# Performance work log

Measured on AMD Instinct MI355X. Metric: run time of the kernel, lower is better.

The kernel has to match this reference:

```python
import jax, jax.numpy as jnp
import numpy as np

B, V, F = 64, 100000, 200000


def setup_inputs() -> dict:
    key = jax.random.key(0)
    k1, k2 = jax.random.split(key)
    verts = jax.random.normal(k1, (B, V, 3), dtype=jnp.float32)
    faces = jax.random.randint(k2, (F, 3), 0, V, dtype=jnp.int64)
    return {"verts": verts, "faces": faces}


def reference(verts, faces):
    # Directed edge list from triangles: each face (i,j,k) contributes
    # edges i<->j, j<->k, k<->i (with multiplicity), shape [6F].
    i, j, k = faces[:, 0], faces[:, 1], faces[:, 2]
    src = jnp.concatenate([i, j, j, k, k, i])
    dst = jnp.concatenate([j, i, k, j, i, k])

    nv = verts.shape[1]
    # Degree (neighbor count) per vertex; guard isolated vertices.
    deg = jnp.zeros((nv,), verts.dtype).at[src].add(1.0)
    deg = jnp.maximum(deg, 1.0)

    # Sum of neighbor positions via scatter-add: [B, V, 3]
    nbr_sum = jnp.zeros_like(verts).at[:, src].add(verts[:, dst])

    # Graph Laplacian: x - mean(neighbors)
    Lx = verts - nbr_sum / deg[None, :, None]

    # Per-vertex L2 norm, then mean over batch and vertices (scalar loss).
    per_vert = jnp.sqrt(jnp.sum(Lx * Lx, axis=-1))
    return per_vert.mean()
```

## Files before the change

### kernel.cpp

```cpp
#include <hip/hip_runtime.h>


#define BB 64
#define VV 100000
#define VP1 (VV + 1)
#define FF 200000
#define BUILD_BLOCKS ((FF + 255) / 256)
#define TR_BLOCKS ((VV + 63) / 64)
#define VBLK ((VV + 255) / 256)
#define NCHUNK (VV / 32)
#define SCALE 80.0f
#define BIAS_W ((512u) | (512u << 10) | (512u << 20))

#define WS_GHIST (448u * 1024u)
#define WS_GCUR (448u * 1024u + 128u)
#define WS_SLOTS (512u * 1024u)
#define WS_VPERM (14u * 1024u * 1024u)
#define WS_T (16u * 1024u * 1024u)

__device__ __forceinline__ int quant10(float x) {
    int qi = (int)rintf(x * SCALE);
    qi = min(max(qi, -511), 511);
    return qi + 512;
}

__global__ __launch_bounds__(256) void build_transpose_kernel(
    const float* __restrict__ verts, const int* __restrict__ faces,
    int* __restrict__ count, int* __restrict__ slots,
    unsigned int* __restrict__ T10) {
    __shared__ unsigned int lds32[64 * 100];
    if (blockIdx.x < BUILD_BLOCKS) {
        int f = blockIdx.x * 256 + threadIdx.x;
        if (f < FF) {
            int i = faces[3 * f + 0];
            int j = faces[3 * f + 1];
            int k = faces[3 * f + 2];
            int p;
            p = atomicAdd(count + i, 2);
            if (p + 1 < 32) *(int2*)(slots + ((size_t)i << 5) + p) = make_int2(j, k);
            p = atomicAdd(count + j, 2);
            if (p + 1 < 32) *(int2*)(slots + ((size_t)j << 5) + p) = make_int2(i, k);
            p = atomicAdd(count + k, 2);
            if (p + 1 < 32) *(int2*)(slots + ((size_t)k << 5) + p) = make_int2(i, j);
        }
    } else {
        int v0 = (blockIdx.x - BUILD_BLOCKS) * 64;
        int nv = min(64, VV - v0);
        int nf = 3 * nv;
        if (blockIdx.x == BUILD_BLOCKS && threadIdx.x < 64) {
            int g = threadIdx.x >> 3, bp = threadIdx.x & 7;
            T10[((size_t)g * VP1 + VV) * 8 + bp] = BIAS_W;
        }
        #pragma unroll
        for (int it = 0; it < 12; ++it) {
            int idx = it * 256 + threadIdx.x;
            int b = idx / 48;
            int q = idx - b * 48;
            if (4 * q < nf) {
                const float4 f4 =
                    *(const float4*)(verts + (size_t)b * (VV * 3) + (size_t)v0 * 3 + 4 * q);
                unsigned int u0 = (unsigned)quant10(f4.x);
                unsigned int u1 = (unsigned)quant10(f4.y);
                unsigned int u2 = (unsigned)quant10(f4.z);
                unsigned int u3 = (unsigned)quant10(f4.w);
                uint2 d;
                d.x = u0 | (u1 << 16);
                d.y = u2 | (u3 << 16);
                *(uint2*)&lds32[b * 100 + 2 * q] = d;
            }
        }
        __syncthreads();
        #pragma unroll
        for (int it = 0; it < 16; ++it) {
            int idx = it * 256 + threadIdx.x;
            int g = idx >> 9;
            int rem = idx & 511;
            int vloc = rem >> 3;
            int bp = rem & 7;
            if (vloc < nv) {
                int b = g * 8 + bp;
                int p0 = 3 * vloc;
                unsigned int dlo = lds32[b * 100 + (p0 >> 1)];
                unsigned int dhi = lds32[b * 100 + ((p0 + 2) >> 1)];
                unsigned long long pair = ((unsigned long long)dhi << 32) | dlo;
                pair >>= 16 * (p0 & 1);
                unsigned int u0 = (unsigned int)(pair & 1023u);
                unsigned int u1 = (unsigned int)((pair >> 16) & 1023u);
                unsigned int u2 = (unsigned int)((pair >> 32) & 1023u);
                T10[((size_t)g * VP1 + v0 + vloc) * 8 + bp] = u0 | (u1 << 10) | (u2 << 20);
            }
        }
    }
}

__global__ __launch_bounds__(256) void hist_kernel(const int* __restrict__ count,
                                                   int* __restrict__ ghist) {
    __shared__ int h[17];
    if (threadIdx.x < 17) h[threadIdx.x] = 0;
    __syncthreads();
    int v = blockIdx.x * 256 + threadIdx.x;
    if (v < VV) atomicAdd(&h[min(count[v], 32) >> 1], 1);
    __syncthreads();
    if (threadIdx.x < 17 && h[threadIdx.x]) atomicAdd(&ghist[threadIdx.x], h[threadIdx.x]);
}

__global__ void scan17_kernel(const int* __restrict__ ghist, int* __restrict__ gcur) {
    if (threadIdx.x == 0) {
        int run = 0;
        for (int u = 0; u < 17; ++u) {
            gcur[u] = run;
            run += ghist[u];
        }
    }
}

__global__ __launch_bounds__(256) void scatter_kernel(const int* __restrict__ count,
                                                      int* __restrict__ gcur,
                                                      unsigned int* __restrict__ vperm) {
    __shared__ int h[17], base[17];
    if (threadIdx.x < 17) h[threadIdx.x] = 0;
    __syncthreads();
    int v = blockIdx.x * 256 + threadIdx.x;
    int u = 0, lpos = 0, deg = 0;
    if (v < VV) {
        deg = count[v];
        u = min(deg, 32) >> 1;
        lpos = atomicAdd(&h[u], 1);
    }
    __syncthreads();
    if (threadIdx.x < 17 && h[threadIdx.x])
        base[threadIdx.x] = atomicAdd(&gcur[threadIdx.x], h[threadIdx.x]);
    __syncthreads();
    if (v < VV)
        vperm[base[u] + lpos] = (unsigned)v | ((unsigned)min(deg, 2047) << 20);
}

__inline__ __device__ float waveReduceSumF(float val) {
    #pragma unroll
    for (int o = 32; o > 0; o >>= 1) val += __shfl_down(val, o, 64);
    return val;
}

#define ACC(col, w)                       \
    {                                     \
        sx##col += (int)((w) & 1023u);    \
        sy##col += (int)(((w) >> 10) & 1023u); \
        sz##col += (int)((w) >> 20);      \
    }

#define LOSSC(col, w)                                            \
    {                                                            \
        float ax = (float)((int)((w) & 1023u) - 512);            \
        float ay = (float)((int)(((w) >> 10) & 1023u) - 512);    \
        float az = (float)((int)((w) >> 20) - 512);              \
        float lx = ax - ((float)sx##col - corr) * invd;          \
        float ly = ay - ((float)sy##col - corr) * invd;          \
        float lz = az - ((float)sz##col - corr) * invd;          \
        acc += sqrtf(lx * lx + ly * ly + lz * lz);               \
    }

__global__ __launch_bounds__(256) void loss_kernel(
    const unsigned int* __restrict__ T10, const unsigned int* __restrict__ vperm,
    const int* __restrict__ slots, float* __restrict__ out) {
    int lane = threadIdx.x & 63;
    int half = lane & 1;
    int vg = lane >> 1;
    int g = blockIdx.x & 7;
    const unsigned int* Tg = T10 + (size_t)g * VP1 * 8;
    int wis = ((blockIdx.x >> 3) << 2) + (threadIdx.x >> 6);
    float acc = 0.f;
    #pragma unroll 1
    for (int k = 0; k < 3; ++k) {
        int c = wis + k * 1044;
        if (c >= NCHUNK) break;
        unsigned int entry = vperm[c * 32 + vg];
        int v = (int)(entry & 0xFFFFFu);
        int deg = (int)(entry >> 20);
        int use = min(deg, 32);
        int mu = use;
        mu = max(mu, __shfl_xor(mu, 2, 64));
        mu = max(mu, __shfl_xor(mu, 4, 64));
        mu = max(mu, __shfl_xor(mu, 8, 64));
        mu = max(mu, __shfl_xor(mu, 16, 64));
        mu = max(mu, __shfl_xor(mu, 32, 64));
        mu = __builtin_amdgcn_readfirstlane(mu);
        int mu4 = (mu + 3) & ~3;
        const int* row = slots + ((size_t)v << 5);
        uint4 selfw = *(const uint4*)(Tg + ((size_t)v << 3) + (half << 2));
        int sx0 = 0, sy0 = 0, sz0 = 0, sx1 = 0, sy1 = 0, sz1 = 0;
        int sx2 = 0, sy2 = 0, sz2 = 0, sx3 = 0, sy3 = 0, sz3 = 0;
        for (int t = 0; t < mu4; t += 4) {
            int2 p01 = *(const int2*)(row + t);
            int2 p23 = *(const int2*)(row + t + 2);
            int n0 = (t + 0 < use) ? p01.x : VV;
            int n1 = (t + 1 < use) ? p01.y : VV;
            int n2 = (t + 2 < use) ? p23.x : VV;
            int n3 = (t + 3 < use) ? p23.y : VV;
            uint4 w0 = *(const uint4*)(Tg + ((size_t)n0 << 3) + (half << 2));
            uint4 w1 = *(const uint4*)(Tg + ((size_t)n1 << 3) + (half << 2));
            uint4 w2 = *(const uint4*)(Tg + ((size_t)n2 << 3) + (half << 2));
            uint4 w3 = *(const uint4*)(Tg + ((size_t)n3 << 3) + (half << 2));
            ACC(0, w0.x) ACC(1, w0.y) ACC(2, w0.z) ACC(3, w0.w)
            ACC(0, w1.x) ACC(1, w1.y) ACC(2, w1.z) ACC(3, w1.w)
            ACC(0, w2.x) ACC(1, w2.y) ACC(2, w2.z) ACC(3, w2.w)
            ACC(0, w3.x) ACC(1, w3.y) ACC(2, w3.z) ACC(3, w3.w)
        }
        float corr = 512.0f * (float)mu4;
        float invd = 1.0f / fmaxf((float)deg, 1.0f);
        LOSSC(0, selfw.x) LOSSC(1, selfw.y) LOSSC(2, selfw.z) LOSSC(3, selfw.w)
    }
    acc = waveReduceSumF(acc);
    __shared__ float wsums[4];
    int wid = threadIdx.x >> 6;
    if ((threadIdx.x & 63) == 0) wsums[wid] = acc;
    __syncthreads();
    if (threadIdx.x == 0) {
        float ssum = wsums[0] + wsums[1] + wsums[2] + wsums[3];
        atomicAdd(out, ssum * (1.0f / (SCALE * (float)BB * (float)VV)));
    }
}

extern "C" void kernel_launch(void* const* d_in, const int* in_sizes, int n_in,
                              void* d_out, int out_size, void* d_ws, size_t ws_size,
                              hipStream_t stream) {
    const float* verts = (const float*)d_in[0];
    const int* faces = (const int*)d_in[1];
    float* out = (float*)d_out;

    int* count = (int*)d_ws;
    int* ghist = (int*)((char*)d_ws + WS_GHIST);
    int* gcur = (int*)((char*)d_ws + WS_GCUR);
    int* slots = (int*)((char*)d_ws + WS_SLOTS);
    unsigned int* vperm = (unsigned int*)((char*)d_ws + WS_VPERM);
    unsigned int* T10 = (unsigned int*)((char*)d_ws + WS_T);

    hipMemsetAsync(d_ws, 0, WS_SLOTS, stream);
    hipMemsetAsync(d_out, 0, sizeof(float), stream);

    build_transpose_kernel<<<BUILD_BLOCKS + TR_BLOCKS, 256, 0, stream>>>(
        verts, faces, count, slots, T10);
    hist_kernel<<<VBLK, 256, 0, stream>>>(count, ghist);
    scan17_kernel<<<1, 64, 0, stream>>>(ghist, gcur);
    scatter_kernel<<<VBLK, 256, 0, stream>>>(count, gcur, vperm);

    loss_kernel<<<2088, 256, 0, stream>>>(T10, vperm, slots, out);
}
```

Before: 239.1 us.

## Build compact degree-sorted adjacency and compute histogram during counting pass

Replaces the fixed 32-slot per-vertex adjacency with a compact CSR-like array laid out in degree-bucket order. Adjacency rows for vertices processed together by the loss kernel then sit contiguously in memory. The degree histogram is maintained incrementally inside the counting kernel, which removes the separate hist and scan kernels and one memset. The cost is an extra fill pass over faces with a second round of atomics, plus 8-byte vperm entries. The loss kernel also skips adjacency loads for padded slots.

```diff
diff --git a/kernel.cpp b/kernel.cpp
--- a/kernel.cpp
+++ b/kernel.cpp
@@ -12,10 +12,12 @@
 #define SCALE 80.0f
 #define BIAS_W ((512u) | (512u << 10) | (512u << 20))
 
-#define WS_GHIST (448u * 1024u)
-#define WS_GCUR (448u * 1024u + 128u)
-#define WS_SLOTS (512u * 1024u)
-#define WS_VPERM (14u * 1024u * 1024u)
+#define WS_CURSOR (512u * 1024u)
+#define WS_GHIST (1024u * 1024u)
+#define WS_GCUR (1024u * 1024u + 128u)
+#define WS_VPERM (2u * 1024u * 1024u)
+#define WS_AOFFV (3u * 1024u * 1024u)
+#define WS_ADJC (4u * 1024u * 1024u)
 #define WS_T (16u * 1024u * 1024u)
 
 __device__ __forceinline__ int quant10(float x) {
@@ -24,26 +26,40 @@
     return qi + 512;
 }
 
-__global__ __launch_bounds__(256) void build_transpose_kernel(
+__global__ __launch_bounds__(256) void count_transpose_kernel(
     const float* __restrict__ verts, const int* __restrict__ faces,
-    int* __restrict__ count, int* __restrict__ slots,
-    unsigned int* __restrict__ T10) {
-    __shared__ unsigned int lds32[64 * 100];
+    int* __restrict__ count, int* __restrict__ ghist,
+    unsigned int* __restrict__ T10, float* __restrict__ out) {
     if (blockIdx.x < BUILD_BLOCKS) {
+        __shared__ int h[17];
+        if (threadIdx.x < 17) h[threadIdx.x] = 0;
+        __syncthreads();
         int f = blockIdx.x * 256 + threadIdx.x;
+        if (f == 0) out[0] = 0.0f;
         if (f < FF) {
-            int i = faces[3 * f + 0];
-            int j = faces[3 * f + 1];
-            int k = faces[3 * f + 2];
-            int p;
-            p = atomicAdd(count + i, 2);
-            if (p + 1 < 32) *(int2*)(slots + ((size_t)i << 5) + p) = make_int2(j, k);
-            p = atomicAdd(count + j, 2);
-            if (p + 1 < 32) *(int2*)(slots + ((size_t)j << 5) + p) = make_int2(i, k);
-            p = atomicAdd(count + k, 2);
-            if (p + 1 < 32) *(int2*)(slots + ((size_t)k << 5) + p) = make_int2(i, j);
+            int vid[3];
+            vid[0] = faces[3 * f + 0];
+            vid[1] = faces[3 * f + 1];
+            vid[2] = faces[3 * f + 2];
+            #pragma unroll
+            for (int e = 0; e < 3; ++e) {
+                int p = atomicAdd(count + vid[e], 2);
+                int uo = min(p >> 1, 16);
+                int un = min((p >> 1) + 1, 16);
+                if (uo != un) {
+                    atomicSub(&h[uo], 1);
+                    atomicAdd(&h[un], 1);
+                }
+            }
+        }
+        __syncthreads();
+        if (threadIdx.x < 17) {
+            int d = h[threadIdx.x];
+            if (blockIdx.x == 0 && threadIdx.x == 0) d += VV;
+            if (d) atomicAdd(&ghist[threadIdx.x], d);
         }
     } else {
+        __shared__ unsigned int lds32[64 * 100];
         int v0 = (blockIdx.x - BUILD_BLOCKS) * 64;
         int nv = min(64, VV - v0);
         int nf = 3 * nv;
@@ -93,32 +109,15 @@
     }
 }
 
-__global__ __launch_bounds__(256) void hist_kernel(const int* __restrict__ count,
-                                                   int* __restrict__ ghist) {
-    __shared__ int h[17];
-    if (threadIdx.x < 17) h[threadIdx.x] = 0;
-    __syncthreads();
-    int v = blockIdx.x * 256 + threadIdx.x;
-    if (v < VV) atomicAdd(&h[min(count[v], 32) >> 1], 1);
-    __syncthreads();
-    if (threadIdx.x < 17 && h[threadIdx.x]) atomicAdd(&ghist[threadIdx.x], h[threadIdx.x]);
-}
-
-__global__ void scan17_kernel(const int* __restrict__ ghist, int* __restrict__ gcur) {
-    if (threadIdx.x == 0) {
-        int run = 0;
-        for (int u = 0; u < 17; ++u) {
-            gcur[u] = run;
-            run += ghist[u];
-        }
-    }
-}
-
-__global__ __launch_bounds__(256) void scatter_kernel(const int* __restrict__ count,
-                                                      int* __restrict__ gcur,
-                                                      unsigned int* __restrict__ vperm) {
-    __shared__ int h[17], base[17];
-    if (threadIdx.x < 17) h[threadIdx.x] = 0;
+__global__ __launch_bounds__(256) void scatter_kernel(
+    const int* __restrict__ count, const int* __restrict__ ghist,
+    int* __restrict__ gcurOff, uint2* __restrict__ vperm2,
+    unsigned int* __restrict__ adjOffByV) {
+    __shared__ int h[17], base[17], sg[17];
+    if (threadIdx.x < 17) {
+        h[threadIdx.x] = 0;
+        sg[threadIdx.x] = ghist[threadIdx.x];
+    }
     __syncthreads();
     int v = blockIdx.x * 256 + threadIdx.x;
     int u = 0, lpos = 0, deg = 0;
@@ -129,10 +128,39 @@
     }
     __syncthreads();
     if (threadIdx.x < 17 && h[threadIdx.x])
-        base[threadIdx.x] = atomicAdd(&gcur[threadIdx.x], h[threadIdx.x]);
-    __syncthreads();
-    if (v < VV)
-        vperm[base[u] + lpos] = (unsigned)v | ((unsigned)min(deg, 2047) << 20);
+        base[threadIdx.x] = atomicAdd(&gcurOff[threadIdx.x], h[threadIdx.x]);
+    __syncthreads();
+    if (v < VV) {
+        int pos = base[u] + lpos;
+        int vstart = 0, astart = 0;
+        for (int t = 0; t < u; ++t) {
+            vstart += sg[t];
+            astart += sg[t] * 2 * t;
+        }
+        unsigned int aoff = (unsigned)(astart + pos * (2 * u));
+        uint2 e;
+        e.x = (unsigned)v | ((unsigned)min(deg, 2047) << 20);
+        e.y = aoff;
+        vperm2[vstart + pos] = e;
+        adjOffByV[v] = aoff;
+    }
+}
+
+__global__ __launch_bounds__(256) void fill_kernel(
+    const int* __restrict__ faces, const unsigned int* __restrict__ adjOffByV,
+    int* __restrict__ cursor, int* __restrict__ adjC) {
+    int f = blockIdx.x * 256 + threadIdx.x;
+    if (f >= FF) return;
+    int i = faces[3 * f + 0];
+    int j = faces[3 * f + 1];
+    int k = faces[3 * f + 2];
+    int p;
+    p = atomicAdd(cursor + i, 2);
+    if (p + 1 < 32) *(int2*)(adjC + adjOffByV[i] + p) = make_int2(j, k);
+    p = atomicAdd(cursor + j, 2);
+    if (p + 1 < 32) *(int2*)(adjC + adjOffByV[j] + p) = make_int2(i, k);
+    p = atomicAdd(cursor + k, 2);
+    if (p + 1 < 32) *(int2*)(adjC + adjOffByV[k] + p) = make_int2(i, j);
 }
 
 __inline__ __device__ float waveReduceSumF(float val) {
@@ -141,27 +169,27 @@
     return val;
 }
 
-#define ACC(col, w)                       \
-    {                                     \
-        sx##col += (int)((w) & 1023u);    \
+#define ACC(col, w)                            \
+    {                                          \
+        sx##col += (int)((w) & 1023u);         \
         sy##col += (int)(((w) >> 10) & 1023u); \
-        sz##col += (int)((w) >> 20);      \
-    }
-
-#define LOSSC(col, w)                                            \
-    {                                                            \
-        float ax = (float)((int)((w) & 1023u) - 512);            \
-        float ay = (float)((int)(((w) >> 10) & 1023u) - 512);    \
-        float az = (float)((int)((w) >> 20) - 512);              \
-        float lx = ax - ((float)sx##col - corr) * invd;          \
-        float ly = ay - ((float)sy##col - corr) * invd;          \
-        float lz = az - ((float)sz##col - corr) * invd;          \
-        acc += sqrtf(lx * lx + ly * ly + lz * lz);               \
+        sz##col += (int)((w) >> 20);           \
+    }
+
+#define LOSSC(col, w)                                         \
+    {                                                         \
+        float ax = (float)((int)((w) & 1023u) - 512);         \
+        float ay = (float)((int)(((w) >> 10) & 1023u) - 512); \
+        float az = (float)((int)((w) >> 20) - 512);           \
+        float lx = ax - ((float)sx##col - corr) * invd;       \
+        float ly = ay - ((float)sy##col - corr) * invd;       \
+        float lz = az - ((float)sz##col - corr) * invd;       \
+        acc += sqrtf(lx * lx + ly * ly + lz * lz);            \
     }
 
 __global__ __launch_bounds__(256) void loss_kernel(
-    const unsigned int* __restrict__ T10, const unsigned int* __restrict__ vperm,
-    const int* __restrict__ slots, float* __restrict__ out) {
+    const unsigned int* __restrict__ T10, const uint2* __restrict__ vperm2,
+    const int* __restrict__ adjC, float* __restrict__ out) {
     int lane = threadIdx.x & 63;
     int half = lane & 1;
     int vg = lane >> 1;
@@ -173,9 +201,9 @@
     for (int k = 0; k < 3; ++k) {
         int c = wis + k * 1044;
         if (c >= NCHUNK) break;
-        unsigned int entry = vperm[c * 32 + vg];
-        int v = (int)(entry & 0xFFFFFu);
-        int deg = (int)(entry >> 20);
+        uint2 entry = vperm2[c * 32 + vg];
+        int v = (int)(entry.x & 0xFFFFFu);
+        int deg = (int)(entry.x >> 20);
         int use = min(deg, 32);
         int mu = use;
         mu = max(mu, __shfl_xor(mu, 2, 64));
@@ -185,17 +213,17 @@
         mu = max(mu, __shfl_xor(mu, 32, 64));
         mu = __builtin_amdgcn_readfirstlane(mu);
         int mu4 = (mu + 3) & ~3;
-        const int* row = slots + ((size_t)v << 5);
+        const int* row = adjC + entry.y;
         uint4 selfw = *(const uint4*)(Tg + ((size_t)v << 3) + (half << 2));
         int sx0 = 0, sy0 = 0, sz0 = 0, sx1 = 0, sy1 = 0, sz1 = 0;
         int sx2 = 0, sy2 = 0, sz2 = 0, sx3 = 0, sy3 = 0, sz3 = 0;
         for (int t = 0; t < mu4; t += 4) {
-            int2 p01 = *(const int2*)(row + t);
-            int2 p23 = *(const int2*)(row + t + 2);
-            int n0 = (t + 0 < use) ? p01.x : VV;
-            int n1 = (t + 1 < use) ? p01.y : VV;
+            int2 p01 = (t + 1 < use) ? *(const int2*)(row + t) : make_int2(VV, VV);
+            int2 p23 = (t + 3 < use) ? *(const int2*)(row + t + 2) : make_int2(VV, VV);
+            int n0 = p01.x;
+            int n1 = p01.y;
             int n2 = (t + 2 < use) ? p23.x : VV;
-            int n3 = (t + 3 < use) ? p23.y : VV;
+            int n3 = p23.y;
             uint4 w0 = *(const uint4*)(Tg + ((size_t)n0 << 3) + (half << 2));
             uint4 w1 = *(const uint4*)(Tg + ((size_t)n1 << 3) + (half << 2));
             uint4 w2 = *(const uint4*)(Tg + ((size_t)n2 << 3) + (half << 2));
@@ -228,20 +256,20 @@
     float* out = (float*)d_out;
 
     int* count = (int*)d_ws;
+    int* cursor = (int*)((char*)d_ws + WS_CURSOR);
     int* ghist = (int*)((char*)d_ws + WS_GHIST);
-    int* gcur = (int*)((char*)d_ws + WS_GCUR);
-    int* slots = (int*)((char*)d_ws + WS_SLOTS);
-    unsigned int* vperm = (unsigned int*)((char*)d_ws + WS_VPERM);
+    int* gcurOff = (int*)((char*)d_ws + WS_GCUR);
+    uint2* vperm2 = (uint2*)((char*)d_ws + WS_VPERM);
+    unsigned int* adjOffByV = (unsigned int*)((char*)d_ws + WS_AOFFV);
+    int* adjC = (int*)((char*)d_ws + WS_ADJC);
     unsigned int* T10 = (unsigned int*)((char*)d_ws + WS_T);
 
-    hipMemsetAsync(d_ws, 0, WS_SLOTS, stream);
-    hipMemsetAsync(d_out, 0, sizeof(float), stream);
-
-    build_transpose_kernel<<<BUILD_BLOCKS + TR_BLOCKS, 256, 0, stream>>>(
-        verts, faces, count, slots, T10);
-    hist_kernel<<<VBLK, 256, 0, stream>>>(count, ghist);
-    scan17_kernel<<<1, 64, 0, stream>>>(ghist, gcur);
-    scatter_kernel<<<VBLK, 256, 0, stream>>>(count, gcur, vperm);
-
-    loss_kernel<<<2088, 256, 0, stream>>>(T10, vperm, slots, out);
-}
+    hipMemsetAsync(d_ws, 0, WS_GHIST + 256u, stream);
+
+    count_transpose_kernel<<<BUILD_BLOCKS + TR_BLOCKS, 256, 0, stream>>>(
+        verts, faces, count, ghist, T10, out);
+    scatter_kernel<<<VBLK, 256, 0, stream>>>(count, ghist, gcurOff, vperm2, adjOffByV);
+    fill_kernel<<<BUILD_BLOCKS, 256, 0, stream>>>(faces, adjOffByV, cursor, adjC);
+
+    loss_kernel<<<2088, 256, 0, stream>>>(T10, vperm2, adjC, out);
+}
```

Result: slower. 253.8 us (+6.2%).
